# Optimization experiments

Hardware: AMD Instinct MI355X
Metric: run time of the kernel (lower is better)

## Reference

```python
import jax, jax.numpy as jnp
import numpy as np

N = 8388608  # batch size
RANGE = 0.02  # self.range in the original module


def setup_inputs() -> dict:
    key = jax.random.key(0)
    k1, k2 = jax.random.split(key)
    preds = jax.random.uniform(k1, (N, 3), dtype=jnp.float32)
    # target is binary ground truth (conditions compare against 0 and 1)
    target = jax.random.randint(k2, (N, 3), 0, 2).astype(jnp.float32)
    return {"preds": preds, "target": target}


def reference(preds, target):
    # Vectorized translation of the per-row scalar branching in RangeLoss.forward.
    p0, p1, p2 = preds[:, 0], preds[:, 1], preds[:, 2]
    t0, t1, t2 = target[:, 0], target[:, 1], target[:, 2]

    # columns 0 and 2: snap target to pred when pred is confidently correct
    t0 = jnp.where((p0 < 0.1) & (t0 == 0.0), p0, t0)
    t0 = jnp.where((p0 > 0.9) & (t0 == 1.0), p0, t0)
    t2 = jnp.where((p2 < 0.1) & (t2 == 0.0), p2, t2)
    t2 = jnp.where((p2 > 0.9) & (t2 == 1.0), p2, t2)

    # column 1: if preds[:,2] > 0.9 take pred; elif pred within +/-RANGE of target take pred
    in_range = (p1 * (1.0 + RANGE) > t1) & (p1 * (1.0 - RANGE) < t1)
    t1 = jnp.where(p2 > 0.9, p1, jnp.where(in_range, p1, t1))

    tgt = jnp.stack([t0, t1, t2], axis=1)  # [N, 3]
    # use_log=False, reduce='mean' in the module defaults
    return jnp.mean((preds - tgt) ** 2)
```

## Files before the change

### kernel.cpp

```cpp
#include <hip/hip_runtime.h>


#define N3      25165824
#define G4      6291456
#define BLOCK   256
#define UNROLL  4
#define NBLOCKS (G4 / (BLOCK * UNROLL))
#define INV_TOTAL (1.0f / 25165824.0f)

__global__ void __launch_bounds__(BLOCK) rangeloss_stage1(
    const float4* __restrict__ preds4,
    const float4* __restrict__ target4,
    const float*  __restrict__ predsf,
    float* __restrict__ partials)
{
    const int base = blockIdx.x * (BLOCK * UNROLL) + threadIdx.x;
    const int lane = threadIdx.x & 63;

    float4 p[UNROLL], t[UNROLL];

    #pragma unroll
    for (int k = 0; k < UNROLL; ++k) {
        const int i = base + k * BLOCK;
        p[k] = preds4[i];
        t[k] = target4[i];
    }

    float sum = 0.0f;

    #pragma unroll
    for (int k = 0; k < UNROLL; ++k) {
        const int i = base + k * BLOCK;

        float pnext = __shfl_down(p[k].x, 1, 64);
        if (lane == 63) {
            const int nf = 4 * i + 4;
            pnext = predsf[nf < N3 ? nf : 0];
        }

        const float pe[4]  = {p[k].x, p[k].y, p[k].z, p[k].w};
        const float te[4]  = {t[k].x, t[k].y, t[k].z, t[k].w};
        const float pnx[4] = {p[k].y, p[k].z, p[k].w, pnext};

        const int c0 = (4 * i) % 3;

        #pragma unroll
        for (int e = 0; e < 4; ++e) {
            int col = c0 + e;
            col = (col >= 3) ? col - 3 : col;

            const float pp = pe[e], tt = te[e];

            const bool rule02 = (pp < 0.1f && tt == 0.0f) || (pp > 0.9f && tt == 1.0f);
            const bool rule1  = (pnx[e] > 0.9f) || (pp * 1.02f > tt && pp * 0.98f < tt);
            const bool snap   = (col == 1) ? rule1 : rule02;

            const float tn = snap ? pp : tt;
            const float d  = pp - tn;
            sum += d * d;
        }
    }

    sum *= INV_TOTAL;

    #pragma unroll
    for (int off = 32; off > 0; off >>= 1)
        sum += __shfl_down(sum, off, 64);

    __shared__ float smem[BLOCK / 64];
    const int wave = threadIdx.x >> 6;
    if (lane == 0) smem[wave] = sum;
    __syncthreads();

    if (threadIdx.x == 0)
        partials[blockIdx.x] = smem[0] + smem[1] + smem[2] + smem[3];
}

__global__ void __launch_bounds__(BLOCK) rangeloss_stage2(
    const float* __restrict__ partials,
    float* __restrict__ out)
{
    float sum = 0.0f;
    for (int i = threadIdx.x; i < NBLOCKS; i += BLOCK)
        sum += partials[i];

    #pragma unroll
    for (int off = 32; off > 0; off >>= 1)
        sum += __shfl_down(sum, off, 64);

    __shared__ float smem[BLOCK / 64];
    const int lane = threadIdx.x & 63;
    const int wave = threadIdx.x >> 6;
    if (lane == 0) smem[wave] = sum;
    __syncthreads();

    if (threadIdx.x == 0)
        out[0] = smem[0] + smem[1] + smem[2] + smem[3];
}

extern "C" void kernel_launch(void* const* d_in, const int* in_sizes, int n_in,
                              void* d_out, int out_size, void* d_ws, size_t ws_size,
                              hipStream_t stream)
{
    const float4* preds4  = (const float4*)d_in[0];
    const float4* target4 = (const float4*)d_in[1];
    const float*  predsf  = (const float*)d_in[0];
    float* partials = (float*)d_ws;
    float* out = (float*)d_out;

    rangeloss_stage1<<<NBLOCKS, BLOCK, 0, stream>>>(preds4, target4, predsf, partials);
    rangeloss_stage2<<<1, BLOCK, 0, stream>>>(partials, out);
}
```

Baseline: 216.7 us.

## Persistent-style blocks with double-buffered loads and nontemporal target reads

```diff
diff --git a/kernel.cpp b/kernel.cpp
--- a/kernel.cpp
+++ b/kernel.cpp
@@ -5,61 +5,83 @@
 #define G4      6291456
 #define BLOCK   256
 #define UNROLL  4
-#define NBLOCKS (G4 / (BLOCK * UNROLL))
+#define NB      1536
+#define NIT     4
+#define CSTRIDE (NB * BLOCK * UNROLL)
 #define INV_TOTAL (1.0f / 25165824.0f)
 
-__global__ void __launch_bounds__(BLOCK) rangeloss_stage1(
-    const float4* __restrict__ preds4,
-    const float4* __restrict__ target4,
-    const float*  __restrict__ predsf,
-    float* __restrict__ partials)
+typedef float vfloat4 __attribute__((ext_vector_type(4)));
+
+struct Chunk {
+    vfloat4 p[UNROLL];
+    vfloat4 t[UNROLL];
+    float   pn[UNROLL];
+};
+
+__device__ __forceinline__ void load_chunk(
+    Chunk& c, int base,
+    const vfloat4* __restrict__ preds4,
+    const vfloat4* __restrict__ target4,
+    const float*   __restrict__ predsf)
 {
-    const int base = blockIdx.x * (BLOCK * UNROLL) + threadIdx.x;
-    const int lane = threadIdx.x & 63;
-
-    float4 p[UNROLL], t[UNROLL];
-
     #pragma unroll
     for (int k = 0; k < UNROLL; ++k) {
         const int i = base + k * BLOCK;
-        p[k] = preds4[i];
-        t[k] = target4[i];
+        c.p[k] = preds4[i];
+        c.t[k] = __builtin_nontemporal_load(&target4[i]);
+        c.pn[k] = predsf[min(4 * i + 4, N3 - 1)];
+    }
+}
+
+__device__ __forceinline__ void compute_chunk(
+    const Chunk& c, const bool is_c1[UNROLL][4], float& sum)
+{
+    #pragma unroll
+    for (int k = 0; k < UNROLL; ++k) {
+        const float pe[4]  = {c.p[k].x, c.p[k].y, c.p[k].z, c.p[k].w};
+        const float te[4]  = {c.t[k].x, c.t[k].y, c.t[k].z, c.t[k].w};
+        const float pnx[4] = {c.p[k].y, c.p[k].z, c.p[k].w, c.pn[k]};
+
+        #pragma unroll
+        for (int e = 0; e < 4; ++e) {
+            const float pp = pe[e], tt = te[e];
+            const bool rule02 = (pp < 0.1f && tt == 0.0f) || (pp > 0.9f && tt == 1.0f);
+            const bool rule1  = (pnx[e] > 0.9f) || (pp * 1.02f > tt && pp * 0.98f < tt);
+            const bool snap   = is_c1[k][e] ? rule1 : rule02;
+            const float d = snap ? 0.0f : (pp - tt);
+            sum += d * d;
+        }
+    }
+}
+
+__global__ void __launch_bounds__(BLOCK) rangeloss_stage1(
+    const vfloat4* __restrict__ preds4,
+    const vfloat4* __restrict__ target4,
+    const float*   __restrict__ predsf,
+    float* __restrict__ partials)
+{
+    const int slot0 = blockIdx.x * (BLOCK * UNROLL) + threadIdx.x;
+
+    bool is_c1[UNROLL][4];
+    #pragma unroll
+    for (int k = 0; k < UNROLL; ++k) {
+        const int ph = (slot0 + k * BLOCK) % 3;
+        #pragma unroll
+        for (int e = 0; e < 4; ++e)
+            is_c1[k][e] = ((ph + e) % 3) == 1;
     }
 
     float sum = 0.0f;
+    Chunk A, B;
+    load_chunk(A, slot0, preds4, target4, predsf);
 
     #pragma unroll
-    for (int k = 0; k < UNROLL; ++k) {
-        const int i = base + k * BLOCK;
-
-        float pnext = __shfl_down(p[k].x, 1, 64);
-        if (lane == 63) {
-            const int nf = 4 * i + 4;
-            pnext = predsf[nf < N3 ? nf : 0];
-        }
-
-        const float pe[4]  = {p[k].x, p[k].y, p[k].z, p[k].w};
-        const float te[4]  = {t[k].x, t[k].y, t[k].z, t[k].w};
-        const float pnx[4] = {p[k].y, p[k].z, p[k].w, pnext};
-
-        const int c0 = (4 * i) % 3;
-
-        #pragma unroll
-        for (int e = 0; e < 4; ++e) {
-            int col = c0 + e;
-            col = (col >= 3) ? col - 3 : col;
-
-            const float pp = pe[e], tt = te[e];
-
-            const bool rule02 = (pp < 0.1f && tt == 0.0f) || (pp > 0.9f && tt == 1.0f);
-            const bool rule1  = (pnx[e] > 0.9f) || (pp * 1.02f > tt && pp * 0.98f < tt);
-            const bool snap   = (col == 1) ? rule1 : rule02;
-
-            const float tn = snap ? pp : tt;
-            const float d  = pp - tn;
-            sum += d * d;
-        }
+    for (int it = 0; it < NIT - 1; ++it) {
+        load_chunk(B, slot0 + (it + 1) * CSTRIDE, preds4, target4, predsf);
+        compute_chunk(A, is_c1, sum);
+        A = B;
     }
+    compute_chunk(A, is_c1, sum);
 
     sum *= INV_TOTAL;
 
@@ -68,6 +90,7 @@
         sum += __shfl_down(sum, off, 64);
 
     __shared__ float smem[BLOCK / 64];
+    const int lane = threadIdx.x & 63;
     const int wave = threadIdx.x >> 6;
     if (lane == 0) smem[wave] = sum;
     __syncthreads();
@@ -81,7 +104,7 @@
     float* __restrict__ out)
 {
     float sum = 0.0f;
-    for (int i = threadIdx.x; i < NBLOCKS; i += BLOCK)
+    for (int i = threadIdx.x; i < NB; i += BLOCK)
         sum += partials[i];
 
     #pragma unroll
@@ -102,12 +125,12 @@
                               void* d_out, int out_size, void* d_ws, size_t ws_size,
                               hipStream_t stream)
 {
-    const float4* preds4  = (const float4*)d_in[0];
-    const float4* target4 = (const float4*)d_in[1];
-    const float*  predsf  = (const float*)d_in[0];
+    const vfloat4* preds4  = (const vfloat4*)d_in[0];
+    const vfloat4* target4 = (const vfloat4*)d_in[1];
+    const float*   predsf  = (const float*)d_in[0];
     float* partials = (float*)d_ws;
     float* out = (float*)d_out;
 
-    rangeloss_stage1<<<NBLOCKS, BLOCK, 0, stream>>>(preds4, target4, predsf, partials);
+    rangeloss_stage1<<<NB, BLOCK, 0, stream>>>(preds4, target4, predsf, partials);
     rangeloss_stage2<<<1, BLOCK, 0, stream>>>(partials, out);
 }
```

After: 204.6 us. -5.6%, faster.
